# Performance work log

Measured on AMD Instinct MI355X. Metric: run time of the kernel, lower is better.

The kernel has to match this reference:

```python
import jax, jax.numpy as jnp
import numpy as np

N, E, D_IN, HID = 100000, 3200000, 256, 128
EPS = 1e-5  # BatchNorm1d default eps


def batchnorm(x, gamma, beta):
    # training-mode BatchNorm1d: batch stats, biased variance
    mu = x.mean(axis=0)
    var = ((x - mu) ** 2).mean(axis=0)
    return (x - mu) * jax.lax.rsqrt(var + EPS) * gamma + beta


def setup_inputs() -> dict:
    key = jax.random.key(0)
    ks = jax.random.split(key, 6)
    s_in = 1.0 / np.sqrt(D_IN)
    s_h = 1.0 / np.sqrt(HID)
    return {
        "x": jax.random.normal(ks[0], (N, D_IN), jnp.float32),
        "edge_index": jax.random.randint(ks[1], (2, E), 0, N),
        "W1": jax.random.uniform(ks[2], (D_IN, HID), jnp.float32, -s_in, s_in),
        "b1": jnp.zeros((HID,), jnp.float32),
        "g1": jnp.ones((HID,), jnp.float32),
        "be1": jnp.zeros((HID,), jnp.float32),
        "Wl": jax.random.uniform(ks[3], (HID, HID), jnp.float32, -s_h, s_h),
        "bl": jnp.zeros((HID,), jnp.float32),
        "Wr": jax.random.uniform(ks[4], (HID, HID), jnp.float32, -s_h, s_h),
        "g2": jnp.ones((HID,), jnp.float32),
        "be2": jnp.zeros((HID,), jnp.float32),
    }


def reference(x, edge_index, W1, b1, g1, be1, Wl, bl, Wr, g2, be2):
    # input_linear: Linear -> BatchNorm1d, then ReLU
    feat = jax.nn.relu(batchnorm(x @ W1 + b1, g1, be1))  # [N, HID]

    # SAGEConv: mean-aggregate source features at destinations
    src, dst = edge_index[0], edge_index[1]
    msg_sum = jax.ops.segment_sum(feat[src], dst, num_segments=N)       # [N, HID]
    deg = jax.ops.segment_sum(jnp.ones((E, 1), feat.dtype), dst, num_segments=N)
    mean = msg_sum / jnp.maximum(deg, 1.0)

    # out = lin_l(aggr) + lin_r(x); lin_l has bias, lin_r does not (PyG default)
    out = mean @ Wl + bl + feat @ Wr
    out_feat = batchnorm(out, g2, be2)
    return feat, out_feat
```

## Files before the change

### kernel.cpp

```cpp
#include <hip/hip_runtime.h>

#define NN 100000
#define NE 3200000
#define KD 256
#define HD 128
#define NB 782
#define CAP 4608

typedef __bf16 bf16x8 __attribute__((ext_vector_type(8)));
typedef float  f32x8  __attribute__((ext_vector_type(8)));
typedef float  f32x4  __attribute__((ext_vector_type(4)));
typedef float  f32x2  __attribute__((ext_vector_type(2)));
typedef unsigned u32x2 __attribute__((ext_vector_type(2)));
typedef unsigned u32x4 __attribute__((ext_vector_type(4)));

__device__ __forceinline__ f32x4 mfma16(bf16x8 a, bf16x8 b, f32x4 c) {
  return __builtin_amdgcn_mfma_f32_16x16x32_bf16(a, b, c, 0, 0, 0);
}

__global__ void prep_w(const float* __restrict__ W1, const float* __restrict__ Wl,
                       const float* __restrict__ Wr, __bf16* __restrict__ Bt1,
                       __bf16* __restrict__ Bt2, float* __restrict__ stats,
                       int* __restrict__ bucket_cur) {
  if (blockIdx.x == 0) {
    for (int i = threadIdx.x; i < 1024; i += 256) stats[i] = 0.f;
  } else if (blockIdx.x == 1) {
    for (int i = threadIdx.x; i < NB; i += 256) bucket_cur[i] = i * CAP;
  }
  int c = blockIdx.x;
  int k = threadIdx.x;
  Bt1[c * KD + k] = (__bf16)W1[k * HD + c];
  float w = (k < HD) ? Wl[k * HD + c] : Wr[(k - HD) * HD + c];
  Bt2[c * KD + k] = (__bf16)w;
}

__global__ __launch_bounds__(1024) void b_scatter(const int* __restrict__ src,
                                                  const int* __restrict__ dst,
                                                  int* __restrict__ bucket_cur,
                                                  unsigned* __restrict__ pairs) {
  __shared__ int h[NB];
  __shared__ int cur[NB];
  __shared__ int gbase[NB];
  for (int i = threadIdx.x; i < NB; i += 1024) { h[i] = 0; cur[i] = 0; }
  __syncthreads();
  int base = blockIdx.x * 12500;
  for (int i = threadIdx.x; i < 12500; i += 1024)
    atomicAdd(&h[dst[base + i] >> 7], 1);
  __syncthreads();
  for (int b = threadIdx.x; b < NB; b += 1024) {
    int c = h[b];
    gbase[b] = c ? atomicAdd(&bucket_cur[b], c) : 0;
  }
  __syncthreads();
  for (int i = threadIdx.x; i < 12500; i += 1024) {
    int d = dst[base + i];
    int s = src[base + i];
    int b = d >> 7;
    int r = atomicAdd(&cur[b], 1);
    pairs[gbase[b] + r] = ((unsigned)s << 7) | (unsigned)(d & 127);
  }
}

__global__ __launch_bounds__(256) void b_sort(const int* __restrict__ bucket_cur,
                                              unsigned* __restrict__ pc,
                                              int* __restrict__ row_start,
                                              int* __restrict__ row_cnt) {
  __shared__ unsigned sin[CAP];
  __shared__ unsigned sout[CAP];
  __shared__ int h[128], ex[128];
  int b = blockIdx.x;
  int n0 = b * CAP;
  int cnt = bucket_cur[b] - n0;
  if (cnt > CAP) cnt = CAP;
  if (threadIdx.x < 128) h[threadIdx.x] = 0;
  __syncthreads();
  for (int i = threadIdx.x; i < cnt; i += 256) {
    unsigned v = pc[n0 + i];
    sin[i] = v;
    atomicAdd(&h[v & 127], 1);
  }
  __syncthreads();
  if (threadIdx.x < 128) ex[threadIdx.x] = h[threadIdx.x];
  __syncthreads();
  for (int off = 1; off < 128; off <<= 1) {
    int u = 0;
    if (threadIdx.x < 128 && threadIdx.x >= off) u = ex[threadIdx.x - off];
    __syncthreads();
    if (threadIdx.x < 128) ex[threadIdx.x] += u;
    __syncthreads();
  }
  if (threadIdx.x < 128) {
    int c = h[threadIdx.x];
    int excl = ex[threadIdx.x] - c;
    int node = b * 128 + threadIdx.x;
    if (node < NN) {
      row_start[node] = n0 + excl;
      row_cnt[node] = c;
    }
    h[threadIdx.x] = excl;
  }
  __syncthreads();
  for (int i = threadIdx.x; i < cnt; i += 256) {
    unsigned v = sin[i];
    int r = atomicAdd(&h[v & 127], 1);
    sout[r] = v >> 7;
  }
  __syncthreads();
  for (int i = threadIdx.x; i < cnt; i += 256)
    pc[n0 + i] = sout[i];
}

__global__ __launch_bounds__(256, 2) void gemm_x(const float* __restrict__ A,
                                                 const __bf16* __restrict__ Bt,
                                                 float* __restrict__ C,
                                                 float* __restrict__ sumc,
                                                 float* __restrict__ sqc) {
  __shared__ __bf16 sB[HD * KD];
  __shared__ float lsum[HD], lsq[HD];
  int tid = threadIdx.x;
  if (tid < HD) { lsum[tid] = 0.f; lsq[tid] = 0.f; }
  for (int i = tid; i < HD * KD / 8; i += 256) {
    int r = i >> 5, g = i & 31;
    bf16x8 v = *(const bf16x8*)(Bt + r * KD + (g << 3));
    *(bf16x8*)(&sB[r * KD + ((g ^ (r & 7)) << 3)]) = v;
  }
  __syncthreads();
  int wave = tid >> 6, lane = tid & 63;
  int q = lane >> 4, m = lane & 15;
  int rowbase = blockIdx.x * 128 + wave * 32;
  f32x4 acc[2][8];
  f32x4 z = {0.f, 0.f, 0.f, 0.f};
#pragma unroll
  for (int s = 0; s < 2; ++s)
#pragma unroll
    for (int t = 0; t < 8; ++t) acc[s][t] = z;
  int r0 = rowbase + m;       if (r0 > NN - 1) r0 = NN - 1;
  int r1 = rowbase + 16 + m;  if (r1 > NN - 1) r1 = NN - 1;
  const float* pa0 = A + (size_t)r0 * KD + q * 8;
  const float* pa1 = A + (size_t)r1 * KD + q * 8;
#pragma unroll
  for (int k0 = 0; k0 < KD; k0 += 32) {
    f32x8 u0 = *(const f32x8*)(pa0 + k0);
    f32x8 u1 = *(const f32x8*)(pa1 + k0);
    bf16x8 a0 = __builtin_convertvector(u0, bf16x8);
    bf16x8 a1 = __builtin_convertvector(u1, bf16x8);
    int gb = (k0 >> 3) + q;
#pragma unroll
    for (int t = 0; t < 8; ++t) {
      int c = t * 16 + m;
      bf16x8 bb = *(const bf16x8*)(&sB[c * KD + ((gb ^ (c & 7)) << 3)]);
      acc[0][t] = mfma16(a0, bb, acc[0][t]);
      acc[1][t] = mfma16(a1, bb, acc[1][t]);
    }
  }
  float ps[8], pq2[8];
#pragma unroll
  for (int t = 0; t < 8; ++t) { ps[t] = 0.f; pq2[t] = 0.f; }
#pragma unroll
  for (int s = 0; s < 2; ++s)
#pragma unroll
    for (int rg = 0; rg < 4; ++rg) {
      int r = rowbase + s * 16 + q * 4 + rg;
      if (r < NN) {
        float* Cr = C + (size_t)r * HD + m;
#pragma unroll
        for (int t = 0; t < 8; ++t) {
          float v = acc[s][t][rg];
          Cr[t * 16] = v;
          ps[t] += v;
          pq2[t] += v * v;
        }
      }
    }
#pragma unroll
  for (int t = 0; t < 8; ++t) {
    atomicAdd(&lsum[t * 16 + m], ps[t]);
    atomicAdd(&lsq[t * 16 + m], pq2[t]);
  }
  __syncthreads();
  if (tid < HD) {
    atomicAdd(&sumc[tid], lsum[tid]);
    atomicAdd(&sqc[tid], lsq[tid]);
  }
}

__global__ __launch_bounds__(256, 2) void gemm_cat(const __bf16* __restrict__ A0,
                                                   const __bf16* __restrict__ A1,
                                                   const __bf16* __restrict__ Bt,
                                                   float* __restrict__ C,
                                                   float* __restrict__ sumc,
                                                   float* __restrict__ sqc) {
  __shared__ __bf16 sB[HD * KD];
  __shared__ float lsum[HD], lsq[HD];
  int tid = threadIdx.x;
  if (tid < HD) { lsum[tid] = 0.f; lsq[tid] = 0.f; }
  for (int i = tid; i < HD * KD / 8; i += 256) {
    int r = i >> 5, g = i & 31;
    bf16x8 v = *(const bf16x8*)(Bt + r * KD + (g << 3));
    *(bf16x8*)(&sB[r * KD + ((g ^ (r & 7)) << 3)]) = v;
  }
  __syncthreads();
  int wave = tid >> 6, lane = tid & 63;
  int q = lane >> 4, m = lane & 15;
  int rowbase = blockIdx.x * 128 + wave * 32;
  f32x4 acc[2][8];
  f32x4 z = {0.f, 0.f, 0.f, 0.f};
#pragma unroll
  for (int s = 0; s < 2; ++s)
#pragma unroll
    for (int t = 0; t < 8; ++t) acc[s][t] = z;
  int r0 = rowbase + m;       if (r0 > NN - 1) r0 = NN - 1;
  int r1 = rowbase + 16 + m;  if (r1 > NN - 1) r1 = NN - 1;
  const __bf16* p00 = A0 + (size_t)r0 * HD + q * 8;
  const __bf16* p01 = A1 + (size_t)r0 * HD + q * 8;
  const __bf16* p10 = A0 + (size_t)r1 * HD + q * 8;
  const __bf16* p11 = A1 + (size_t)r1 * HD + q * 8;
#pragma unroll
  for (int k0 = 0; k0 < KD; k0 += 32) {
    int kk = k0 & (HD - 1);
    bf16x8 a0 = (k0 < HD) ? *(const bf16x8*)(p00 + kk) : *(const bf16x8*)(p01 + kk);
    bf16x8 a1 = (k0 < HD) ? *(const bf16x8*)(p10 + kk) : *(const bf16x8*)(p11 + kk);
    int gb = (k0 >> 3) + q;
#pragma unroll
    for (int t = 0; t < 8; ++t) {
      int c = t * 16 + m;
      bf16x8 bb = *(const bf16x8*)(&sB[c * KD + ((gb ^ (c & 7)) << 3)]);
      acc[0][t] = mfma16(a0, bb, acc[0][t]);
      acc[1][t] = mfma16(a1, bb, acc[1][t]);
    }
  }
  float ps[8], pq2[8];
#pragma unroll
  for (int t = 0; t < 8; ++t) { ps[t] = 0.f; pq2[t] = 0.f; }
#pragma unroll
  for (int s = 0; s < 2; ++s)
#pragma unroll
    for (int rg = 0; rg < 4; ++rg) {
      int r = rowbase + s * 16 + q * 4 + rg;
      if (r < NN) {
        float* Cr = C + (size_t)r * HD + m;
#pragma unroll
        for (int t = 0; t < 8; ++t) {
          float v = acc[s][t][rg];
          Cr[t * 16] = v;
          ps[t] += v;
          pq2[t] += v * v;
        }
      }
    }
#pragma unroll
  for (int t = 0; t < 8; ++t) {
    atomicAdd(&lsum[t * 16 + m], ps[t]);
    atomicAdd(&lsq[t * 16 + m], pq2[t]);
  }
  __syncthreads();
  if (tid < HD) {
    atomicAdd(&sumc[tid], lsum[tid]);
    atomicAdd(&sqc[tid], lsq[tid]);
  }
}

__global__ __launch_bounds__(256) void bn_apply(const float* __restrict__ X,
                                                const float* __restrict__ sumc,
                                                const float* __restrict__ sqc,
                                                const float* __restrict__ g,
                                                const float* __restrict__ be,
                                                float* __restrict__ outf,
                                                __bf16* __restrict__ outb,
                                                unsigned char* __restrict__ outq,
                                                int relu) {
  __shared__ float sc[HD], sh[HD];
  if (threadIdx.x < HD) {
    int c = threadIdx.x;
    float mu = sumc[c] * (1.0f / NN);
    float var = sqc[c] * (1.0f / NN) - mu * mu;
    float rs = rsqrtf(var + 1e-5f);
    float a = rs * g[c];
    sc[c] = a;
    sh[c] = be[c] - mu * a;
  }
  __syncthreads();
  size_t base = ((size_t)blockIdx.x * 256 + threadIdx.x) * 8;
  int c0 = (int)(base & (HD - 1));
  f32x4 x0 = *(const f32x4*)(X + base);
  f32x4 x1 = *(const f32x4*)(X + base + 4);
  float o[8];
#pragma unroll
  for (int j = 0; j < 8; ++j) {
    float xv = (j < 4) ? x0[j] : x1[j - 4];
    float v = xv * sc[c0 + j] + sh[c0 + j];
    if (relu) v = fmaxf(v, 0.f);
    o[j] = v;
  }
  f32x4 o0 = {o[0], o[1], o[2], o[3]};
  f32x4 o1 = {o[4], o[5], o[6], o[7]};
  *(f32x4*)(outf + base) = o0;
  *(f32x4*)(outf + base + 4) = o1;
  if (outb) {
    bf16x8 ob;
#pragma unroll
    for (int j = 0; j < 8; ++j) ob[j] = (__bf16)o[j];
    *(bf16x8*)(outb + base) = ob;
    int w0 = 0, w1 = 0;
    w0 = __builtin_amdgcn_cvt_pk_fp8_f32(o[0], o[1], w0, false);
    w0 = __builtin_amdgcn_cvt_pk_fp8_f32(o[2], o[3], w0, true);
    w1 = __builtin_amdgcn_cvt_pk_fp8_f32(o[4], o[5], w1, false);
    w1 = __builtin_amdgcn_cvt_pk_fp8_f32(o[6], o[7], w1, true);
    u32x2 qv = {(unsigned)w0, (unsigned)w1};
    *(u32x2*)(outq + base) = qv;
  }
}

__global__ __launch_bounds__(256) void aggregate(const int* __restrict__ row_start,
                                                 const int* __restrict__ row_cnt,
                                                 const unsigned* __restrict__ csr,
                                                 const unsigned char* __restrict__ featq,
                                                 __bf16* __restrict__ meanb) {
  int node = blockIdx.x * 4 + (threadIdx.x >> 6);
  if (node >= NN) return;
  int lane = threadIdx.x & 63;
  int sub = lane >> 3;
  int m = lane & 7;
  int s = row_start[node];
  int deg = row_cnt[node];
  int e = s + deg;
  f32x2 acc[8];
#pragma unroll
  for (int j = 0; j < 8; ++j) acc[j] = (f32x2){0.f, 0.f};
  const u32x4* rows = (const u32x4*)featq;
  for (int base = s; base < e; base += 64) {
    int nb = e - base;
    if (nb > 64) nb = 64;
    unsigned my = 0;
    if (lane < nb) my = csr[base + lane];
#pragma unroll
    for (int t = 0; t < 64; t += 8) {
      int slot = t + sub;
      unsigned sn = __shfl(my, slot, 64);
      if (slot < nb) {
        u32x4 v = rows[(size_t)sn * 8 + m];
        acc[0] += __builtin_amdgcn_cvt_pk_f32_fp8((int)v.x, false);
        acc[1] += __builtin_amdgcn_cvt_pk_f32_fp8((int)v.x, true);
        acc[2] += __builtin_amdgcn_cvt_pk_f32_fp8((int)v.y, false);
        acc[3] += __builtin_amdgcn_cvt_pk_f32_fp8((int)v.y, true);
        acc[4] += __builtin_amdgcn_cvt_pk_f32_fp8((int)v.z, false);
        acc[5] += __builtin_amdgcn_cvt_pk_f32_fp8((int)v.z, true);
        acc[6] += __builtin_amdgcn_cvt_pk_f32_fp8((int)v.w, false);
        acc[7] += __builtin_amdgcn_cvt_pk_f32_fp8((int)v.w, true);
      }
    }
  }
#pragma unroll
  for (int j = 0; j < 8; ++j) {
    acc[j].x += __shfl_xor(acc[j].x, 8, 64);
    acc[j].y += __shfl_xor(acc[j].y, 8, 64);
    acc[j].x += __shfl_xor(acc[j].x, 16, 64);
    acc[j].y += __shfl_xor(acc[j].y, 16, 64);
    acc[j].x += __shfl_xor(acc[j].x, 32, 64);
    acc[j].y += __shfl_xor(acc[j].y, 32, 64);
  }
  if (sub == 0) {
    float inv = 1.0f / (float)(deg < 1 ? 1 : deg);
    bf16x8 o0, o1;
#pragma unroll
    for (int j = 0; j < 4; ++j) {
      o0[2 * j]     = (__bf16)(acc[j].x * inv);
      o0[2 * j + 1] = (__bf16)(acc[j].y * inv);
      o1[2 * j]     = (__bf16)(acc[4 + j].x * inv);
      o1[2 * j + 1] = (__bf16)(acc[4 + j].y * inv);
    }
    __bf16* dst = meanb + (size_t)node * HD + m * 16;
    *(bf16x8*)dst = o0;
    *(bf16x8*)(dst + 8) = o1;
  }
}

extern "C" void kernel_launch(void* const* d_in, const int* in_sizes, int n_in,
                              void* d_out, int out_size, void* d_ws, size_t ws_size,
                              hipStream_t stream) {
  (void)in_sizes; (void)n_in; (void)out_size; (void)ws_size;
  const float* x   = (const float*)d_in[0];
  const int*   ei  = (const int*)d_in[1];
  const float* W1  = (const float*)d_in[2];
  const float* g1  = (const float*)d_in[4];
  const float* be1 = (const float*)d_in[5];
  const float* Wl  = (const float*)d_in[6];
  const float* Wr  = (const float*)d_in[8];
  const float* g2  = (const float*)d_in[9];
  const float* be2 = (const float*)d_in[10];

  float* feat_out = (float*)d_out;
  float* out_feat = feat_out + (size_t)NN * HD;
  unsigned char* featq = (unsigned char*)out_feat;

  char* w = (char*)d_ws;
  float*    h          = (float*)(w);
  __bf16*   featb      = (__bf16*)(w + 51200000);
  __bf16*   meanb      = (__bf16*)(w + 76800000);
  unsigned* pc         = (unsigned*)(w + 102400000);
  int*      row_start  = (int*)(w + 116814848);
  int*      row_cnt    = (int*)(w + 117214848);
  int*      bucket_cur = (int*)(w + 117614848);
  float*    stats      = (float*)(w + 117618944);
  __bf16*   Bt1        = (__bf16*)(w + 117623040);
  __bf16*   Bt2        = (__bf16*)(w + 117688576);

  float* sum1 = stats,       * sq1 = stats + 128;
  float* sum2 = stats + 512, * sq2 = stats + 640;

  const int* esrc = ei;
  const int* edst = ei + NE;

  prep_w<<<128, 256, 0, stream>>>(W1, Wl, Wr, Bt1, Bt2, stats, bucket_cur);
  b_scatter<<<256, 1024, 0, stream>>>(esrc, edst, bucket_cur, pc);
  b_sort<<<NB, 256, 0, stream>>>(bucket_cur, pc, row_start, row_cnt);

  gemm_x<<<782, 256, 0, stream>>>(x, Bt1, h, sum1, sq1);
  bn_apply<<<6250, 256, 0, stream>>>(h, sum1, sq1, g1, be1, feat_out, featb, featq, 1);

  aggregate<<<25000, 256, 0, stream>>>(row_start, row_cnt, pc, featq, meanb);

  gemm_cat<<<782, 256, 0, stream>>>(meanb, featb, Bt2, h, sum2, sq2);
  bn_apply<<<6250, 256, 0, stream>>>(h, sum2, sq2, g2, be2, out_feat,
                                     (__bf16*)nullptr, (unsigned char*)nullptr, 0);
}
```

Before: 472.7 us.

## Split GEMM output columns across block pairs and prefetch A tiles in registers

Both dense GEMM kernels now give each block a 256-row by 64-column tile instead of 128 rows by 128 columns. This halves the shared B footprint (32 KB), so occupancy can be raised to 4 blocks per CU. The A-row loads are software-prefetched one k-step ahead into registers, and the first A load is issued before the B staging loop to overlap global latency. In exchange, each A row is now read by two blocks (column halves), doubling A global traffic unless L2 absorbs it.

```diff
diff --git a/kernel.cpp b/kernel.cpp
--- a/kernel.cpp
+++ b/kernel.cpp
@@ -110,62 +110,73 @@
     pc[n0 + i] = sout[i];
 }
 
-__global__ __launch_bounds__(256, 2) void gemm_x(const float* __restrict__ A,
+__global__ __launch_bounds__(256, 4) void gemm_x(const float* __restrict__ A,
                                                  const __bf16* __restrict__ Bt,
                                                  float* __restrict__ C,
                                                  float* __restrict__ sumc,
                                                  float* __restrict__ sqc) {
-  __shared__ __bf16 sB[HD * KD];
-  __shared__ float lsum[HD], lsq[HD];
+  __shared__ __bf16 sB[64 * KD];
+  __shared__ float lsum[64], lsq[64];
   int tid = threadIdx.x;
-  if (tid < HD) { lsum[tid] = 0.f; lsq[tid] = 0.f; }
-  for (int i = tid; i < HD * KD / 8; i += 256) {
-    int r = i >> 5, g = i & 31;
-    bf16x8 v = *(const bf16x8*)(Bt + r * KD + (g << 3));
-    *(bf16x8*)(&sB[r * KD + ((g ^ (r & 7)) << 3)]) = v;
-  }
-  __syncthreads();
+  int colbase = (blockIdx.x & 1) * 64;
+  int rowtile = blockIdx.x >> 1;
+  if (tid < 64) { lsum[tid] = 0.f; lsq[tid] = 0.f; }
   int wave = tid >> 6, lane = tid & 63;
   int q = lane >> 4, m = lane & 15;
-  int rowbase = blockIdx.x * 128 + wave * 32;
-  f32x4 acc[2][8];
+  int rowbase = rowtile * 256 + wave * 64;
+  const float* pa[4];
+#pragma unroll
+  for (int g = 0; g < 4; ++g) {
+    int r = rowbase + g * 16 + m;
+    if (r > NN - 1) r = NN - 1;
+    pa[g] = A + (size_t)r * KD + q * 8;
+  }
+  f32x8 u[4];
+#pragma unroll
+  for (int g = 0; g < 4; ++g) u[g] = *(const f32x8*)(pa[g]);
+  for (int i = tid; i < 64 * KD / 8; i += 256) {
+    int r = i >> 5, g = i & 31;
+    bf16x8 v = *(const bf16x8*)(Bt + (size_t)(colbase + r) * KD + (g << 3));
+    *(bf16x8*)(&sB[r * KD + ((g ^ (r & 7)) << 3)]) = v;
+  }
+  f32x4 acc[4][4];
   f32x4 z = {0.f, 0.f, 0.f, 0.f};
 #pragma unroll
-  for (int s = 0; s < 2; ++s)
-#pragma unroll
-    for (int t = 0; t < 8; ++t) acc[s][t] = z;
-  int r0 = rowbase + m;       if (r0 > NN - 1) r0 = NN - 1;
-  int r1 = rowbase + 16 + m;  if (r1 > NN - 1) r1 = NN - 1;
-  const float* pa0 = A + (size_t)r0 * KD + q * 8;
-  const float* pa1 = A + (size_t)r1 * KD + q * 8;
+  for (int g = 0; g < 4; ++g)
+#pragma unroll
+    for (int t = 0; t < 4; ++t) acc[g][t] = z;
+  __syncthreads();
 #pragma unroll
   for (int k0 = 0; k0 < KD; k0 += 32) {
-    f32x8 u0 = *(const f32x8*)(pa0 + k0);
-    f32x8 u1 = *(const f32x8*)(pa1 + k0);
-    bf16x8 a0 = __builtin_convertvector(u0, bf16x8);
-    bf16x8 a1 = __builtin_convertvector(u1, bf16x8);
+    bf16x8 a[4];
+#pragma unroll
+    for (int g = 0; g < 4; ++g) a[g] = __builtin_convertvector(u[g], bf16x8);
+    if (k0 + 32 < KD) {
+#pragma unroll
+      for (int g = 0; g < 4; ++g) u[g] = *(const f32x8*)(pa[g] + k0 + 32);
+    }
     int gb = (k0 >> 3) + q;
 #pragma unroll
-    for (int t = 0; t < 8; ++t) {
+    for (int t = 0; t < 4; ++t) {
       int c = t * 16 + m;
       bf16x8 bb = *(const bf16x8*)(&sB[c * KD + ((gb ^ (c & 7)) << 3)]);
-      acc[0][t] = mfma16(a0, bb, acc[0][t]);
-      acc[1][t] = mfma16(a1, bb, acc[1][t]);
-    }
-  }
-  float ps[8], pq2[8];
-#pragma unroll
-  for (int t = 0; t < 8; ++t) { ps[t] = 0.f; pq2[t] = 0.f; }
-#pragma unroll
-  for (int s = 0; s < 2; ++s)
+#pragma unroll
+      for (int g = 0; g < 4; ++g) acc[g][t] = mfma16(a[g], bb, acc[g][t]);
+    }
+  }
+  float ps[4], pq2[4];
+#pragma unroll
+  for (int t = 0; t < 4; ++t) { ps[t] = 0.f; pq2[t] = 0.f; }
+#pragma unroll
+  for (int g = 0; g < 4; ++g)
 #pragma unroll
     for (int rg = 0; rg < 4; ++rg) {
-      int r = rowbase + s * 16 + q * 4 + rg;
+      int r = rowbase + g * 16 + q * 4 + rg;
       if (r < NN) {
-        float* Cr = C + (size_t)r * HD + m;
-#pragma unroll
-        for (int t = 0; t < 8; ++t) {
-          float v = acc[s][t][rg];
+        float* Cr = C + (size_t)r * HD + colbase + m;
+#pragma unroll
+        for (int t = 0; t < 4; ++t) {
+          float v = acc[g][t][rg];
           Cr[t * 16] = v;
           ps[t] += v;
           pq2[t] += v * v;
@@ -173,75 +184,91 @@
       }
     }
 #pragma unroll
-  for (int t = 0; t < 8; ++t) {
+  for (int t = 0; t < 4; ++t) {
     atomicAdd(&lsum[t * 16 + m], ps[t]);
     atomicAdd(&lsq[t * 16 + m], pq2[t]);
   }
   __syncthreads();
-  if (tid < HD) {
-    atomicAdd(&sumc[tid], lsum[tid]);
-    atomicAdd(&sqc[tid], lsq[tid]);
-  }
-}
-
-__global__ __launch_bounds__(256, 2) void gemm_cat(const __bf16* __restrict__ A0,
+  if (tid < 64) {
+    atomicAdd(&sumc[colbase + tid], lsum[tid]);
+    atomicAdd(&sqc[colbase + tid], lsq[tid]);
+  }
+}
+
+__global__ __launch_bounds__(256, 4) void gemm_cat(const __bf16* __restrict__ A0,
                                                    const __bf16* __restrict__ A1,
                                                    const __bf16* __restrict__ Bt,
                                                    float* __restrict__ C,
                                                    float* __restrict__ sumc,
                                                    float* __restrict__ sqc) {
-  __shared__ __bf16 sB[HD * KD];
-  __shared__ float lsum[HD], lsq[HD];
+  __shared__ __bf16 sB[64 * KD];
+  __shared__ float lsum[64], lsq[64];
   int tid = threadIdx.x;
-  if (tid < HD) { lsum[tid] = 0.f; lsq[tid] = 0.f; }
-  for (int i = tid; i < HD * KD / 8; i += 256) {
-    int r = i >> 5, g = i & 31;
-    bf16x8 v = *(const bf16x8*)(Bt + r * KD + (g << 3));
-    *(bf16x8*)(&sB[r * KD + ((g ^ (r & 7)) << 3)]) = v;
-  }
-  __syncthreads();
+  int colbase = (blockIdx.x & 1) * 64;
+  int rowtile = blockIdx.x >> 1;
+  if (tid < 64) { lsum[tid] = 0.f; lsq[tid] = 0.f; }
   int wave = tid >> 6, lane = tid & 63;
   int q = lane >> 4, m = lane & 15;
-  int rowbase = blockIdx.x * 128 + wave * 32;
-  f32x4 acc[2][8];
+  int rowbase = rowtile * 256 + wave * 64;
+  const __bf16* p0[4];
+  const __bf16* p1[4];
+#pragma unroll
+  for (int g = 0; g < 4; ++g) {
+    int r = rowbase + g * 16 + m;
+    if (r > NN - 1) r = NN - 1;
+    p0[g] = A0 + (size_t)r * HD + q * 8;
+    p1[g] = A1 + (size_t)r * HD + q * 8;
+  }
+  bf16x8 u[4];
+#pragma unroll
+  for (int g = 0; g < 4; ++g) u[g] = *(const bf16x8*)(p0[g]);
+  for (int i = tid; i < 64 * KD / 8; i += 256) {
+    int r = i >> 5, g = i & 31;
+    bf16x8 v = *(const bf16x8*)(Bt + (size_t)(colbase + r) * KD + (g << 3));
+    *(bf16x8*)(&sB[r * KD + ((g ^ (r & 7)) << 3)]) = v;
+  }
+  f32x4 acc[4][4];
   f32x4 z = {0.f, 0.f, 0.f, 0.f};
 #pragma unroll
-  for (int s = 0; s < 2; ++s)
-#pragma unroll
-    for (int t = 0; t < 8; ++t) acc[s][t] = z;
-  int r0 = rowbase + m;       if (r0 > NN - 1) r0 = NN - 1;
-  int r1 = rowbase + 16 + m;  if (r1 > NN - 1) r1 = NN - 1;
-  const __bf16* p00 = A0 + (size_t)r0 * HD + q * 8;
-  const __bf16* p01 = A1 + (size_t)r0 * HD + q * 8;
-  const __bf16* p10 = A0 + (size_t)r1 * HD + q * 8;
-  const __bf16* p11 = A1 + (size_t)r1 * HD + q * 8;
+  for (int g = 0; g < 4; ++g)
+#pragma unroll
+    for (int t = 0; t < 4; ++t) acc[g][t] = z;
+  __syncthreads();
 #pragma unroll
   for (int k0 = 0; k0 < KD; k0 += 32) {
-    int kk = k0 & (HD - 1);
-    bf16x8 a0 = (k0 < HD) ? *(const bf16x8*)(p00 + kk) : *(const bf16x8*)(p01 + kk);
-    bf16x8 a1 = (k0 < HD) ? *(const bf16x8*)(p10 + kk) : *(const bf16x8*)(p11 + kk);
+    bf16x8 a[4];
+#pragma unroll
+    for (int g = 0; g < 4; ++g) a[g] = u[g];
+    int kn = k0 + 32;
+    if (kn < KD) {
+      int kk = kn & (HD - 1);
+#pragma unroll
+      for (int g = 0; g < 4; ++g)
+        u[g] = (kn < HD) ? *(const bf16x8*)(p0[g] + kk)
+                         : *(const bf16x8*)(p1[g] + kk);
+    }
     int gb = (k0 >> 3) + q;
 #pragma unroll
-    for (int t = 0; t < 8; ++t) {
+    for (int t = 0; t < 4; ++t) {
       int c = t * 16 + m;
       bf16x8 bb = *(const bf16x8*)(&sB[c * KD + ((gb ^ (c & 7)) << 3)]);
-      acc[0][t] = mfma16(a0, bb, acc[0][t]);
-      acc[1][t] = mfma16(a1, bb, acc[1][t]);
-    }
-  }
-  float ps[8], pq2[8];
-#pragma unroll
-  for (int t = 0; t < 8; ++t) { ps[t] = 0.f; pq2[t] = 0.f; }
-#pragma unroll
-  for (int s = 0; s < 2; ++s)
+#pragma unroll
+      for (int g = 0; g < 4; ++g) acc[g][t] = mfma16(a[g], bb, acc[g][t]);
+    }
+  }
+  float ps[4], pq2[4];
+#pragma unroll
+  for (int t = 0; t < 4; ++t) { ps[t] = 0.f; pq2[t] = 0.f; }
+#pragma unroll
+  for (int g = 0; g < 4; ++g)
 #pragma unroll
     for (int rg = 0; rg < 4; ++rg) {
-      int r = rowbase + s * 16 + q * 4 + rg;
+      int r = rowbase + g * 16 + q * 4 + rg;
       if (r < NN) {
-        float* Cr = C + (size_t)r * HD + m;
-#pragma unroll
-        for (int t = 0; t < 8; ++t) {
-          float v = acc[s][t][rg];
+        float* Cr = C + (size_t)r * HD + colbase + m;
+#pragma unroll
+        for (int t = 0; t < 4; ++t) {
+          float v = acc[g][t][rg];
           Cr[t * 16] = v;
           ps[t] += v;
           pq2[t] += v * v;
@@ -249,14 +276,14 @@
       }
     }
 #pragma unroll
-  for (int t = 0; t < 8; ++t) {
+  for (int t = 0; t < 4; ++t) {
     atomicAdd(&lsum[t * 16 + m], ps[t]);
     atomicAdd(&lsq[t * 16 + m], pq2[t]);
   }
   __syncthreads();
-  if (tid < HD) {
-    atomicAdd(&sumc[tid], lsum[tid]);
-    atomicAdd(&sqc[tid], lsq[tid]);
+  if (tid < 64) {
+    atomicAdd(&sumc[colbase + tid], lsum[tid]);
+    atomicAdd(&sqc[colbase + tid], lsq[tid]);
   }
 }
 
```

Result: faster. 449.5 us (-4.9%).
